# Optimization experiments

Measured on AMD Instinct MI355X. Metric: run time of the kernel, lower is better.

The kernel has to match this reference:

```python
import jax, jax.numpy as jnp
import numpy as np

B, T, L = 64, 60, 49
EMBED, HID, VOCAB = 768, 768, 10000


def setup_inputs() -> dict:
    key = jax.random.key(0)
    ks = jax.random.split(key, 17)
    def n(k, shape, s=1.0):
        return jax.random.normal(k, shape, dtype=jnp.float32) * s
    W = 0.02  # param init scale
    return {
        "x": n(ks[0], (B, T, 2 * EMBED)),
        "hiddens": n(ks[1], (B, T, HID)),
        "cells": n(ks[2], (B, T, HID)),
        "G": n(ks[3], (B, L, HID)),
        "H": n(ks[4], (B, L, HID)),
        # Sentinel params (bias=False)
        "W_sx": n(ks[5], (HID, 2 * EMBED), W),
        "W_sh": n(ks[6], (HID, HID), W),
        # SwitchableAttention params
        "W_ax": n(ks[7], (HID, 2 * EMBED), W),
        "W_ah": n(ks[8], (HID, HID), W),
        "W_ag": n(ks[9], (HID, HID), W),
        "w_switch": n(ks[10], (1, HID), W),
        # Atten (adaptive attention) params, bias=False
        "Wv": n(ks[11], (L, HID), W),
        "Wg": n(ks[12], (L, HID), W),
        "Ws": n(ks[13], (L, HID), W),
        "wh": n(ks[14], (1, L), W),
        # output MLP
        "W_mlp": n(ks[15], (VOCAB, HID), W),
        "b_mlp": jnp.zeros((VOCAB,), dtype=jnp.float32),
    }


def reference(x, hiddens, cells, G, H, W_sx, W_sh, W_ax, W_ah, W_ag,
              w_switch, Wv, Wg, Ws, wh, W_mlp, b_mlp):
    # Dropout layers are treated as identity (eval mode).
    b, t, _ = x.shape
    # h_{t-1}: zero initial hidden prepended, last step dropped
    h0 = jnp.zeros((b, 1, HID), dtype=hiddens.dtype)
    hiddens_t_1 = jnp.concatenate([h0, hiddens[:, :-1, :]], axis=1)

    # Sentinel gate: sigmoid(Wx x + Wh h_{t-1}) * tanh(c_t)
    gate = jax.nn.sigmoid(jnp.einsum('bte,he->bth', x, W_sx)
                          + jnp.einsum('btk,hk->bth', hiddens_t_1, W_sh))
    s_t = gate * jnp.tanh(cells)  # [B,T,HID]

    # SwitchableAttention: gate between visual H and guidance G per region,
    # conditioned on pooled word context x.
    q = jnp.einsum('bte,he->bth', x, W_ax).mean(axis=1)  # [B,HID]
    sH = jnp.einsum('blh,oh->blo', jnp.tanh(jnp.einsum('blh,kh->blk', H, W_ah) + q[:, None, :]), w_switch)  # [B,L,1]
    sG = jnp.einsum('blh,oh->blo', jnp.tanh(jnp.einsum('blh,kh->blk', G, W_ag) + q[:, None, :]), w_switch)  # [B,L,1]
    switch_weights = jax.nn.softmax(jnp.concatenate([sH, sG], axis=-1), axis=-1)  # [B,L,2]
    V = switch_weights[..., 0:1] * H + switch_weights[..., 1:2] * G  # [B,L,HID]

    # Adaptive attention (Atten): spatial attention + visual sentinel
    pv = jnp.einsum('blh,kh->blk', V, Wv)        # [B,L,49]
    pg = jnp.einsum('bth,kh->btk', hiddens, Wg)  # [B,T,49]
    z_t = jnp.einsum('btlk,ok->btlo', jnp.tanh(pv[:, None, :, :] + pg[:, :, None, :]), wh)[..., 0]  # [B,T,L]
    alpha = jax.nn.softmax(z_t, axis=-1)  # [B,T,L]
    z_s = jnp.einsum('btk,ok->bto', jnp.tanh(jnp.einsum('bth,kh->btk', s_t, Ws) + pg), wh)  # [B,T,1]
    alpha_hat = jax.nn.softmax(jnp.concatenate([z_t, z_s], axis=-1), axis=-1)  # [B,T,L+1]
    beta = alpha_hat[..., -1:]  # [B,T,1]
    c_t = jnp.einsum('btl,blh->bth', alpha, V)
    c_hat = beta * s_t + (1.0 - beta) * c_t

    scores = jnp.einsum('bth,vh->btv', c_hat + hiddens, W_mlp) + b_mlp  # [B,T,VOCAB]
    return scores, alpha, beta, switch_weights
```

## Files before the change

kernel.cpp:

```cpp
#include <hip/hip_runtime.h>

#define BB 64
#define TT 60
#define LL 49
#define HID 768
#define E2 1536
#define VOC 10000
#define BT (BB*TT)
#define BL (BB*LL)
#define NPAD_MLP 10240
#define NPAD_S 128

typedef __bf16 bf16x8 __attribute__((ext_vector_type(8)));
typedef float f32x4 __attribute__((ext_vector_type(4)));

__device__ __forceinline__ unsigned short f2bf(float f) {
  union { float f; unsigned int u; } v; v.f = f;
  unsigned int u = v.u;
  return (unsigned short)((u + 0x7fffu + ((u >> 16) & 1u)) >> 16);
}
__device__ __forceinline__ float bf2f(unsigned short h) {
  union { unsigned int u; float f; } v; v.u = ((unsigned int)h) << 16;
  return v.f;
}
__device__ __forceinline__ float fast_tanh(float x) {
  float e = __expf(2.f * x);
  return 1.f - 2.f / (e + 1.f);
}
__device__ __forceinline__ float fast_sigmoid(float x) {
  return 1.f / (1.f + __expf(-x));
}

#define NSEG 14
#define CHUNK4 2048
struct SegT {
  const float* src;
  unsigned short* dst;
  int n4;
  int nrows;
  int mode;
  int blk0;
};
struct SegTable { SegT s[NSEG]; };

__global__ __launch_bounds__(256) void k_convall(SegTable tab) {
  int b = blockIdx.x;
  int si = 0;
#pragma unroll
  for (int i = 1; i < NSEG; ++i) si += (b >= tab.s[i].blk0);
  SegT sg = tab.s[si];
  int lb = b - sg.blk0;
  int end = (lb + 1) * CHUNK4; end = end < sg.n4 ? end : sg.n4;
  for (int i = lb * CHUNK4 + threadIdx.x; i < end; i += 256) {
    ushort4 o; o.x = o.y = o.z = o.w = 0;
    if (sg.mode == 0) {
      float4 v = ((const float4*)sg.src)[i];
      o.x = f2bf(v.x); o.y = f2bf(v.y); o.z = f2bf(v.z); o.w = f2bf(v.w);
    } else if (sg.mode == 1) {
      int row = i / 192;
      if (row < sg.nrows) {
        float4 v = ((const float4*)sg.src)[i];
        o.x = f2bf(v.x); o.y = f2bf(v.y); o.z = f2bf(v.z); o.w = f2bf(v.w);
      }
    } else {
      int bt = i / 192;
      if (bt % TT != 0) {
        float4 v = ((const float4*)sg.src)[i - 192];
        o.x = f2bf(v.x); o.y = f2bf(v.y); o.z = f2bf(v.z); o.w = f2bf(v.w);
      }
    }
    ((ushort4*)sg.dst)[i] = o;
  }
}

__global__ __launch_bounds__(256) void k_xmean(const float* __restrict__ x,
                                               unsigned short* __restrict__ xm) {
  int b = blockIdx.x / 6;
  int c = (blockIdx.x % 6) * 256 + threadIdx.x;
  float s = 0.f;
  for (int t = 0; t < TT; ++t) s += x[((size_t)b * TT + t) * E2 + c];
  xm[(size_t)b * E2 + c] = f2bf(s * (1.f / 60.f));
}

struct SSeg {
  const unsigned short* A; const unsigned short* B; float* C;
  int M, Nout, K, nMblk, blk0;
};
#define NSSEG 3
struct SSegTable { SSeg s[NSSEG]; };

__global__ __launch_bounds__(256) void gemm_bt_seg(SSegTable tab)
{
  __shared__ __attribute__((aligned(16))) unsigned short As[128*32];
  __shared__ __attribute__((aligned(16))) unsigned short Bs[128*32];
  const int tid  = threadIdx.x;
  const int lane = tid & 63;
  const int wave = tid >> 6;

  const int nwg = gridDim.x;
  const int id  = blockIdx.x;
  const int q = nwg >> 3, r = nwg & 7;
  const int xcd = id & 7, lo = id >> 3;
  const int wgid = (xcd < r ? xcd * (q + 1) : r * (q + 1) + (xcd - r) * q) + lo;

  int si = 0;
#pragma unroll
  for (int i = 1; i < NSSEG; ++i) si += (wgid >= tab.s[i].blk0);
  const SSeg sg = tab.s[si];
  const int lwg = wgid - sg.blk0;
  const int mb = lwg % sg.nMblk;
  const int nb = lwg / sg.nMblk;
  const int M = sg.M, Nout = sg.Nout, K = sg.K;
  const unsigned short* __restrict__ A  = sg.A;
  const unsigned short* __restrict__ Bw = sg.B;
  float* __restrict__ C = sg.C;
  const int m0 = mb * 128;
  const int n0 = nb * 128;
  const int wm = (wave >> 1) * 64;
  const int wn = (wave & 1) * 64;

  f32x4 acc[4][4];
#pragma unroll
  for (int i = 0; i < 4; ++i)
#pragma unroll
    for (int j = 0; j < 4; ++j) acc[i][j] = f32x4{0.f, 0.f, 0.f, 0.f};

  const int lrow = lane & 15;
  const int kb   = (lane >> 4) * 8;

  for (int k0 = 0; k0 < K; k0 += 32) {
    __syncthreads();
#pragma unroll
    for (int p = 0; p < 2; ++p) {
      int slot = p * 256 + wave * 64 + lane;
      int row = slot >> 2, c8 = slot & 3;
      int ar = m0 + row; ar = ar < M ? ar : (M - 1);
      const unsigned short* asrc = A + (size_t)ar * K + k0 + c8 * 8;
      __builtin_amdgcn_global_load_lds(
          (const __attribute__((address_space(1))) void*)asrc,
          (__attribute__((address_space(3))) void*)&As[(p * 256 + wave * 64) * 8],
          16, 0, 0);
      const unsigned short* bsrc = Bw + (size_t)(n0 + row) * K + k0 + c8 * 8;
      __builtin_amdgcn_global_load_lds(
          (const __attribute__((address_space(1))) void*)bsrc,
          (__attribute__((address_space(3))) void*)&Bs[(p * 256 + wave * 64) * 8],
          16, 0, 0);
    }
    __syncthreads();

    bf16x8 av[4], bv[4];
#pragma unroll
    for (int i = 0; i < 4; ++i)
      av[i] = *(const bf16x8*)&As[(wm + i * 16 + lrow) * 32 + kb];
#pragma unroll
    for (int j = 0; j < 4; ++j)
      bv[j] = *(const bf16x8*)&Bs[(wn + j * 16 + lrow) * 32 + kb];
#pragma unroll
    for (int i = 0; i < 4; ++i)
#pragma unroll
      for (int j = 0; j < 4; ++j)
        acc[i][j] = __builtin_amdgcn_mfma_f32_16x16x32_bf16(av[i], bv[j], acc[i][j], 0, 0, 0);
  }

  const int cr = (lane >> 4) * 4;
  const int cc = lane & 15;
#pragma unroll
  for (int i = 0; i < 4; ++i) {
    int row0 = m0 + wm + i * 16 + cr;
#pragma unroll
    for (int j = 0; j < 4; ++j) {
      int col = n0 + wn + j * 16 + cc;
      if (col < Nout) {
#pragma unroll
        for (int r2 = 0; r2 < 4; ++r2) {
          int row = row0 + r2;
          if (row < M) C[(size_t)row * Nout + col] = acc[i][j][r2];
        }
      }
    }
  }
}

#define BARR() do { asm volatile("" ::: "memory"); __builtin_amdgcn_s_barrier(); \
                    asm volatile("" ::: "memory"); } while (0)
#define VM2() asm volatile("s_waitcnt vmcnt(2)" ::: "memory")
#define VM0() asm volatile("s_waitcnt vmcnt(0)" ::: "memory")

#define STAGE_OP(ct, op, kt) do {                                               \
  int k0_ = (kt) * 32;                                                          \
  _Pragma("unroll")                                                             \
  for (int l_ = 0; l_ < 2; ++l_) {                                              \
    int rr_ = l_ * 128 + sr0;                                                   \
    int ss_ = ssp ^ ((rr_ >> 1) & 3);                                           \
    int gr_ = (op) ? (n0 + rr_) : ((m0 + rr_) < M ? (m0 + rr_) : (M - 1));      \
    const unsigned short* src_ = ((op) ? Bw : Ap) + (size_t)gr_ * K + k0_ + ss_ * 8; \
    char* dst_ = smem + (ct) * 32768 + (op) * 16384 + l_ * 8192 + w * 1024;     \
    __builtin_amdgcn_global_load_lds(                                           \
        (const __attribute__((address_space(1))) void*)src_,                    \
        (__attribute__((address_space(3))) void*)dst_, 16, 0, 0);               \
  }                                                                             \
} while (0)

#define PHASE(c, JH, STAGE_STMT, VM_STMT) do {                                  \
  if ((JH) == 0) {                                                              \
    _Pragma("unroll")                                                           \
    for (int i_ = 0; i_ < 8; ++i_) {                                            \
      int rr_ = wm + i_ * 16 + lrow;                                            \
      int sp_ = cg ^ ((rr_ >> 1) & 3);                                          \
      afr[i_] = *(const bf16x8*)(smem + (c) * 32768 + rr_ * 64 + sp_ * 16);     \
    }                                                                           \
  }                                                                             \
  {                                                                             \
    int rb0_ = wn + ((JH) * 2) * 16 + lrow;                                     \
    int sb0_ = cg ^ ((rb0_ >> 1) & 3);                                          \
    bfr0 = *(const bf16x8*)(smem + (c) * 32768 + 16384 + rb0_ * 64 + sb0_ * 16); \
    int rb1_ = wn + ((JH) * 2 + 1) * 16 + lrow;                                 \
    int sb1_ = cg ^ ((rb1_ >> 1) & 3);                                          \
    bfr1 = *(const bf16x8*)(smem + (c) * 32768 + 16384 + rb1_ * 64 + sb1_ * 16); \
  }                                                                             \
  STAGE_STMT;                                                                   \
  BARR();                                                                       \
  asm volatile("s_waitcnt lgkmcnt(0)" ::: "memory");                            \
  __builtin_amdgcn_sched_barrier(0);                                            \
  __builtin_amdgcn_s_setprio(1);                                                \
  _Pragma("unroll")                                                             \
  for (int i_ = 0; i_ < 8; ++i_) {                                              \
    acc[i_][(JH) * 2]     = __builtin_amdgcn_mfma_f32_16x16x32_bf16(afr[i_], bfr0, acc[i_][(JH) * 2], 0, 0, 0);     \
    acc[i_][(JH) * 2 + 1] = __builtin_amdgcn_mfma_f32_16x16x32_bf16(afr[i_], bfr1, acc[i_][(JH) * 2 + 1], 0, 0, 0); \
  }                                                                             \
  __builtin_amdgcn_s_setprio(0);                                                \
  VM_STMT;                                                                      \
  BARR();                                                                       \
} while (0)

struct GSeg {
  const unsigned short* A; const unsigned short* B; float* C;
  const float* bias;
  int M, Nout, K, nMblk, blk0;
};
#define NGSEG 5
struct GSegTable { GSeg s[NGSEG]; };

__global__ __launch_bounds__(512, 2) void gemm8p(GSegTable tab)
{
  extern __shared__ char smem[];
  const int tid  = threadIdx.x;
  const int lane = tid & 63;
  const int w    = tid >> 6;
  const int lrow = lane & 15;
  const int cg   = lane >> 4;
  const int sr0  = w * 16 + (lane >> 2);
  const int ssp  = lane & 3;

  const int nwg = gridDim.x;
  const int id  = blockIdx.x;
  const int q = nwg >> 3, r = nwg & 7;
  const int xcd = id & 7, lo = id >> 3;
  const int wgid = (xcd < r ? xcd * (q + 1) : r * (q + 1) + (xcd - r) * q) + lo;

  int si = 0;
#pragma unroll
  for (int i = 1; i < NGSEG; ++i) si += (wgid >= tab.s[i].blk0);
  const GSeg sg = tab.s[si];
  const int lwg = wgid - sg.blk0;
  const int mb = lwg % sg.nMblk;
  const int nb = lwg / sg.nMblk;
  const int M = sg.M, Nout = sg.Nout, K = sg.K;
  const unsigned short* __restrict__ Ap = sg.A;
  const unsigned short* __restrict__ Bw = sg.B;
  float* __restrict__ C = sg.C;
  const float* __restrict__ bias = sg.bias;

  const int m0 = mb * 256;
  const int n0 = nb * 256;
  const int wm = (w >> 2) * 128;
  const int wn = (w & 3) * 64;

  f32x4 acc[8][4];
#pragma unroll
  for (int i = 0; i < 8; ++i)
#pragma unroll
    for (int j = 0; j < 4; ++j) acc[i][j] = f32x4{0.f, 0.f, 0.f, 0.f};
  bf16x8 afr[8];
  bf16x8 bfr0, bfr1;

  const int NT = K >> 5;

  STAGE_OP(0, 0, 0);
  STAGE_OP(0, 1, 0);
  STAGE_OP(1, 0, 1);
  VM2();
  BARR();

  for (int kt = 0; kt < NT - 2; ++kt) {
    const int c = kt & 1;
    PHASE(c, 0, STAGE_OP(c ^ 1, 1, kt + 1), ;);
    PHASE(c, 1, STAGE_OP(c, 0, kt + 2), VM2(););
  }
  {
    const int kt = NT - 2;
    const int c = kt & 1;
    PHASE(c, 0, STAGE_OP(c ^ 1, 1, NT - 1), ;);
    PHASE(c, 1, ;, VM0(););
  }
  {
    const int c = (NT - 1) & 1;
    PHASE(c, 0, ;, ;);
    PHASE(c, 1, ;, ;);
  }

#pragma unroll
  for (int i = 0; i < 8; ++i) {
    int row0 = m0 + wm + i * 16 + (lane >> 4) * 4;
#pragma unroll
    for (int j = 0; j < 4; ++j) {
      int col = n0 + wn + j * 16 + (lane & 15);
      if (col < Nout) {
        float badd = bias ? bias[col] : 0.f;
#pragma unroll
        for (int r2 = 0; r2 < 4; ++r2) {
          int row = row0 + r2;
          if (row < M) C[(size_t)row * Nout + col] = acc[i][j][r2] + badd;
        }
      }
    }
  }
}

__global__ void k_st(const float* __restrict__ XS, const float* __restrict__ HS,
                     const float* __restrict__ cells, unsigned short* __restrict__ stbf, int n) {
  int i = blockIdx.x * blockDim.x + threadIdx.x;
  int stride = gridDim.x * blockDim.x;
  for (; i < n; i += stride) {
    float pre = XS[i] + HS[i];
    float v = fast_sigmoid(pre) * fast_tanh(cells[i]);
    stbf[i] = f2bf(v);
  }
}

__global__ __launch_bounds__(256) void k_switch(
    const float* __restrict__ AH, const float* __restrict__ AG,
    const float* __restrict__ q, const float* __restrict__ wsw,
    const float* __restrict__ H, const float* __restrict__ G,
    unsigned short* __restrict__ Vbf, float* __restrict__ sw_out)
{
  int bl = blockIdx.x;
  int b = bl / LL;
  int tid = threadIdx.x;
  float aH = 0.f, aG = 0.f;
  for (int h = tid; h < HID; h += 256) {
    float qv = q[b * HID + h], w = wsw[h];
    aH += fast_tanh(AH[(size_t)bl * HID + h] + qv) * w;
    aG += fast_tanh(AG[(size_t)bl * HID + h] + qv) * w;
  }
#pragma unroll
  for (int off = 32; off > 0; off >>= 1) {
    aH += __shfl_down(aH, off);
    aG += __shfl_down(aG, off);
  }
  __shared__ float redH[4], redG[4];
  int lane = tid & 63, wave = tid >> 6;
  if (lane == 0) { redH[wave] = aH; redG[wave] = aG; }
  __syncthreads();
  float sH = redH[0] + redH[1] + redH[2] + redH[3];
  float sG = redG[0] + redG[1] + redG[2] + redG[3];
  float m = fmaxf(sH, sG);
  float e0 = __expf(sH - m), e1 = __expf(sG - m);
  float inv = 1.f / (e0 + e1);
  float sw0 = e0 * inv, sw1 = e1 * inv;
  if (tid == 0) { sw_out[bl * 2] = sw0; sw_out[bl * 2 + 1] = sw1; }
  for (int h = tid; h < HID; h += 256) {
    float v = sw0 * H[(size_t)bl * HID + h] + sw1 * G[(size_t)bl * HID + h];
    Vbf[(size_t)bl * HID + h] = f2bf(v);
  }
}

__global__ __launch_bounds__(256) void k_attn(
    const float* __restrict__ PV, const float* __restrict__ PG,
    const float* __restrict__ SS, const float* __restrict__ wh,
    const unsigned short* __restrict__ stbf, const unsigned short* __restrict__ Vbf,
    const float* __restrict__ hiddens,
    float* __restrict__ alpha_out, float* __restrict__ beta_out,
    unsigned short* __restrict__ chh)
{
  const int TG = 4;
  int b  = blockIdx.x / (TT / TG);
  int t0 = (blockIdx.x % (TT / TG)) * TG;
  int tid = threadIdx.x;
  __shared__ float pg_s[TG][LL], wh_s[LL], zz[TG][LL + 1], alpha_s[TG][LL], beta_sh[TG];

  if (tid < LL) wh_s[tid] = wh[tid];
  if (tid < TG * LL) {
    int tt = tid / LL, k = tid - tt * LL;
    pg_s[tt][k] = PG[(size_t)(b * TT + t0 + tt) * 64 + k];
  }
  __syncthreads();

  if (tid < TG * (LL + 1)) {
    int tt = tid / (LL + 1), l = tid - tt * (LL + 1);
    const float* src = (l < LL) ? &PV[((size_t)b * LL + l) * 64]
                                : &SS[(size_t)(b * TT + t0 + tt) * 64];
    float acc = 0.f;
    for (int k = 0; k < LL; ++k) acc += fast_tanh(src[k] + pg_s[tt][k]) * wh_s[k];
    zz[tt][l] = acc;
  }
  __syncthreads();

  if (tid < TG) {
    int tt = tid, bt = b * TT + t0 + tt;
    float mx = -1e30f;
    for (int l = 0; l < LL; ++l) mx = fmaxf(mx, zz[tt][l]);
    float sum = 0.f;
    for (int l = 0; l < LL; ++l) { float e = __expf(zz[tt][l] - mx); alpha_s[tt][l] = e; sum += e; }
    float inv = 1.f / sum;
    for (int l = 0; l < LL; ++l) {
      alpha_s[tt][l] *= inv;
      alpha_out[(size_t)bt * LL + l] = alpha_s[tt][l];
    }
    float mx2 = fmaxf(mx, zz[tt][LL]);
    float s2 = 0.f;
    for (int l = 0; l <= LL; ++l) s2 += __expf(zz[tt][l] - mx2);
    float bet = __expf(zz[tt][LL] - mx2) / s2;
    beta_sh[tt] = bet;
    beta_out[bt] = bet;
  }
  __syncthreads();

  for (int h = tid; h < HID; h += 256) {
    float ct[TG] = {0.f, 0.f, 0.f, 0.f};
    for (int l = 0; l < LL; ++l) {
      float v = bf2f(Vbf[((size_t)b * LL + l) * HID + h]);
#pragma unroll
      for (int tt = 0; tt < TG; ++tt) ct[tt] += alpha_s[tt][l] * v;
    }
#pragma unroll
    for (int tt = 0; tt < TG; ++tt) {
      int bt = b * TT + t0 + tt;
      float bet = beta_sh[tt];
      float s = bf2f(stbf[(size_t)bt * HID + h]);
      float chat = bet * s + (1.f - bet) * ct[tt];
      chh[(size_t)bt * HID + h] = f2bf(chat + hiddens[(size_t)bt * HID + h]);
    }
  }
}

static inline int nblk(long n) {
  long g = (n + 255) / 256;
  if (g > 8192) g = 8192;
  return (int)g;
}

extern "C" void kernel_launch(void* const* d_in, const int* in_sizes, int n_in,
                              void* d_out, int out_size, void* d_ws, size_t ws_size,
                              hipStream_t stream)
{
  const float* x       = (const float*)d_in[0];
  const float* hiddens = (const float*)d_in[1];
  const float* cells   = (const float*)d_in[2];
  const float* G       = (const float*)d_in[3];
  const float* H       = (const float*)d_in[4];
  const float* W_sx    = (const float*)d_in[5];
  const float* W_sh    = (const float*)d_in[6];
  const float* W_ax    = (const float*)d_in[7];
  const float* W_ah    = (const float*)d_in[8];
  const float* W_ag    = (const float*)d_in[9];
  const float* w_sw    = (const float*)d_in[10];
  const float* Wv      = (const float*)d_in[11];
  const float* Wg      = (const float*)d_in[12];
  const float* Ws      = (const float*)d_in[13];
  const float* wh      = (const float*)d_in[14];
  const float* W_mlp   = (const float*)d_in[15];
  const float* b_mlp   = (const float*)d_in[16];

  float* scores = (float*)d_out;
  float* alpha  = scores + (size_t)BT * VOC;
  float* beta   = alpha + (size_t)BT * LL;
  float* swout  = beta + BT;

  char* wsp = (char*)d_ws;
  size_t off = 0;
  auto alloc = [&](size_t bytes) -> char* {
    char* p = wsp + off;
    off += (bytes + 255) & ~(size_t)255;
    return p;
  };

  unsigned short* xbf    = (unsigned short*)alloc((size_t)BT * E2 * 2);
  unsigned short* wsa    = (unsigned short*)alloc((size_t)E2 * E2 * 2);
  unsigned short* hprev  = (unsigned short*)alloc((size_t)BT * HID * 2);
  unsigned short* wshb   = (unsigned short*)alloc((size_t)HID * HID * 2);
  unsigned short* wahb   = (unsigned short*)alloc((size_t)HID * HID * 2);
  unsigned short* wagb   = (unsigned short*)alloc((size_t)HID * HID * 2);
  unsigned short* Hbf    = (unsigned short*)alloc((size_t)BL * HID * 2);
  unsigned short* Gbf    = (unsigned short*)alloc((size_t)BL * HID * 2);
  unsigned short* hidbf  = (unsigned short*)alloc((size_t)BT * HID * 2);
  unsigned short* wvb    = (unsigned short*)alloc((size_t)NPAD_S * HID * 2);
  unsigned short* wgb    = (unsigned short*)alloc((size_t)NPAD_S * HID * 2);
  unsigned short* wsb    = (unsigned short*)alloc((size_t)NPAD_S * HID * 2);
  unsigned short* wmlpb  = (unsigned short*)alloc((size_t)NPAD_MLP * HID * 2);
  unsigned short* Vbf    = (unsigned short*)alloc((size_t)BL * HID * 2);
  unsigned short* stbf   = (unsigned short*)alloc((size_t)BT * HID * 2);
  unsigned short* chh    = (unsigned short*)alloc((size_t)BT * HID * 2);
  unsigned short* xmbf   = (unsigned short*)alloc((size_t)BB * E2 * 2);
  float* XS = (float*)alloc((size_t)BT * HID * 4);
  float* HS = (float*)alloc((size_t)BT * HID * 4);
  float* AH = (float*)alloc((size_t)BL * HID * 4);
  float* AG = (float*)alloc((size_t)BL * HID * 4);
  float* qb = (float*)alloc((size_t)BB * HID * 4);
  float* PV = (float*)alloc((size_t)BL * 64 * 4);
  float* PG = (float*)alloc((size_t)BT * 64 * 4);
  float* SS = (float*)alloc((size_t)BT * 64 * 4);
  (void)ws_size; (void)in_sizes; (void)n_in; (void)out_size;

  SegTable tab;
  int blk = 0, si = 0;
  auto seg = [&](const float* s, unsigned short* d, int n4, int nrows, int mode) {
    tab.s[si].src = s; tab.s[si].dst = d; tab.s[si].n4 = n4;
    tab.s[si].nrows = nrows; tab.s[si].mode = mode; tab.s[si].blk0 = blk;
    blk += (n4 + CHUNK4 - 1) / CHUNK4; ++si;
  };
  seg(W_sx, wsa,                        HID * E2 / 4, 0, 0);
  seg(W_ax, wsa + (size_t)HID * E2,     HID * E2 / 4, 0, 0);
  seg(x, xbf,                           BT * E2 / 4, 0, 0);
  seg(hiddens, hprev,                   BT * HID / 4, 0, 2);
  seg(W_sh, wshb,                       HID * HID / 4, 0, 0);
  seg(W_ah, wahb,                       HID * HID / 4, 0, 0);
  seg(W_ag, wagb,                       HID * HID / 4, 0, 0);
  seg(H, Hbf,                           BL * HID / 4, 0, 0);
  seg(G, Gbf,                           BL * HID / 4, 0, 0);
  seg(hiddens, hidbf,                   BT * HID / 4, 0, 0);
  seg(Wv, wvb,                          NPAD_S * HID / 4, LL, 1);
  seg(Wg, wgb,                          NPAD_S * HID / 4, LL, 1);
  seg(Ws, wsb,                          NPAD_S * HID / 4, LL, 1);
  seg(W_mlp, wmlpb,                     NPAD_MLP * HID / 4, VOC, 1);
  k_convall<<<blk, 256, 0, stream>>>(tab);

  k_xmean<<<BB * 6, 256, 0, stream>>>(x, xmbf);

  GSegTable gt;
  int gblk = 0, gi = 0;
  auto gseg = [&](const unsigned short* A, const unsigned short* B, float* C,
                  const float* bias, int M, int N, int K, int nMblk, int nNblk) {
    gt.s[gi].A = A; gt.s[gi].B = B; gt.s[gi].C = C; gt.s[gi].bias = bias;
    gt.s[gi].M = M; gt.s[gi].Nout = N; gt.s[gi].K = K; gt.s[gi].nMblk = nMblk;
    gt.s[gi].blk0 = gblk;
    gblk += nMblk * nNblk; ++gi;
  };
  gseg(xbf,   wsa,                      XS, nullptr, BT, HID, E2,  15, 3);
  gseg(hprev, wshb,                     HS, nullptr, BT, HID, HID, 15, 3);
  gseg(Hbf,   wahb,                     AH, nullptr, BL, HID, HID, 13, 3);
  gseg(Gbf,   wagb,                     AG, nullptr, BL, HID, HID, 13, 3);
  gseg(xmbf,  wsa + (size_t)HID * E2,   qb, nullptr, BB, HID, E2,  1,  3);
  gemm8p<<<gblk, 512, 65536, stream>>>(gt);

  k_st<<<nblk((long)BT * HID), 256, 0, stream>>>(XS, HS, cells, stbf, BT * HID);
  k_switch<<<BL, 256, 0, stream>>>(AH, AG, qb, w_sw, H, G, Vbf, swout);

  SSegTable st;
  st.s[0] = SSeg{Vbf,   wvb, PV, BL, 64, HID, 25, 0};
  st.s[1] = SSeg{hidbf, wgb, PG, BT, 64, HID, 30, 25};
  st.s[2] = SSeg{stbf,  wsb, SS, BT, 64, HID, 30, 55};
  gemm_bt_seg<<<85, 256, 0, stream>>>(st);

  k_attn<<<BB * (TT / 4), 256, 0, stream>>>(PV, PG, SS, wh, stbf, Vbf, hiddens,
                                            alpha, beta, chh);

  GSegTable gs;
  for (int i = 0; i < NGSEG; ++i) { gs.s[i] = gt.s[i]; gs.s[i].blk0 = 0x7fffffff; }
  gs.s[0] = GSeg{chh, wmlpb, scores, b_mlp, BT, VOC, HID, 15, 0};
  gemm8p<<<15 * 40, 512, 65536, stream>>>(gs);
}
```

Baseline: 311.3 us.

## Switch gemm8p to triple-buffered LDS pipeline with templated row clamping

Moves the main GEMM kernel from a double-buffered to a triple-buffered shared-memory pipeline. Both A and B tiles are now prefetched two k-steps ahead, the wait count is relaxed, and one barrier per phase is dropped. A template flag removes the row clamp and bounds check for the MLP GEMM, whose M is an exact multiple of the tile. Shared memory per block grows to 96KB, which may limit how many blocks fit per CU despite the two-block launch bound.

```diff
diff --git a/kernel.cpp b/kernel.cpp
--- a/kernel.cpp
+++ b/kernel.cpp
@@ -183,50 +183,54 @@
 
 #define BARR() do { asm volatile("" ::: "memory"); __builtin_amdgcn_s_barrier(); \
                     asm volatile("" ::: "memory"); } while (0)
-#define VM2() asm volatile("s_waitcnt vmcnt(2)" ::: "memory")
+#define VM4() asm volatile("s_waitcnt vmcnt(4)" ::: "memory")
 #define VM0() asm volatile("s_waitcnt vmcnt(0)" ::: "memory")
 
-#define STAGE_OP(ct, op, kt) do {                                               \
+#define STAGE1(bufi, op, kt) do {                                               \
   int k0_ = (kt) * 32;                                                          \
   _Pragma("unroll")                                                             \
   for (int l_ = 0; l_ < 2; ++l_) {                                              \
     int rr_ = l_ * 128 + sr0;                                                   \
     int ss_ = ssp ^ ((rr_ >> 1) & 3);                                           \
-    int gr_ = (op) ? (n0 + rr_) : ((m0 + rr_) < M ? (m0 + rr_) : (M - 1));      \
+    int gr_;                                                                    \
+    if (op) gr_ = n0 + rr_;                                                     \
+    else    gr_ = CLAMP ? ((m0 + rr_) < M ? (m0 + rr_) : (M - 1)) : (m0 + rr_); \
     const unsigned short* src_ = ((op) ? Bw : Ap) + (size_t)gr_ * K + k0_ + ss_ * 8; \
-    char* dst_ = smem + (ct) * 32768 + (op) * 16384 + l_ * 8192 + w * 1024;     \
+    char* dst_ = smem + (bufi) * 32768 + (op) * 16384 + l_ * 8192 + w * 1024;   \
     __builtin_amdgcn_global_load_lds(                                           \
         (const __attribute__((address_space(1))) void*)src_,                    \
         (__attribute__((address_space(3))) void*)dst_, 16, 0, 0);               \
   }                                                                             \
 } while (0)
 
-#define PHASE(c, JH, STAGE_STMT, VM_STMT) do {                                  \
-  if ((JH) == 0) {                                                              \
-    _Pragma("unroll")                                                           \
-    for (int i_ = 0; i_ < 8; ++i_) {                                            \
-      int rr_ = wm + i_ * 16 + lrow;                                            \
-      int sp_ = cg ^ ((rr_ >> 1) & 3);                                          \
-      afr[i_] = *(const bf16x8*)(smem + (c) * 32768 + rr_ * 64 + sp_ * 16);     \
-    }                                                                           \
-  }                                                                             \
-  {                                                                             \
-    int rb0_ = wn + ((JH) * 2) * 16 + lrow;                                     \
-    int sb0_ = cg ^ ((rb0_ >> 1) & 3);                                          \
-    bfr0 = *(const bf16x8*)(smem + (c) * 32768 + 16384 + rb0_ * 64 + sb0_ * 16); \
-    int rb1_ = wn + ((JH) * 2 + 1) * 16 + lrow;                                 \
-    int sb1_ = cg ^ ((rb1_ >> 1) & 3);                                          \
-    bfr1 = *(const bf16x8*)(smem + (c) * 32768 + 16384 + rb1_ * 64 + sb1_ * 16); \
-  }                                                                             \
+#define LDA(bufi, row) (*(const bf16x8*)(smem + (bufi) * 32768 + (row) * 64 + (cg ^ (((row) >> 1) & 3)) * 16))
+#define LDB(bufi, row) (*(const bf16x8*)(smem + (bufi) * 32768 + 16384 + (row) * 64 + (cg ^ (((row) >> 1) & 3)) * 16))
+
+#define PH0(bufi, STAGE_STMT) do {                                              \
   STAGE_STMT;                                                                   \
-  BARR();                                                                       \
-  asm volatile("s_waitcnt lgkmcnt(0)" ::: "memory");                            \
-  __builtin_amdgcn_sched_barrier(0);                                            \
+  bfr0 = LDB(bufi, wn + lrow);                                                  \
+  bfr1 = LDB(bufi, wn + 16 + lrow);                                             \
+  _Pragma("unroll")                                                             \
+  for (int i_ = 0; i_ < 8; ++i_) afr[i_] = LDA(bufi, wm + i_ * 16 + lrow);      \
   __builtin_amdgcn_s_setprio(1);                                                \
   _Pragma("unroll")                                                             \
   for (int i_ = 0; i_ < 8; ++i_) {                                              \
-    acc[i_][(JH) * 2]     = __builtin_amdgcn_mfma_f32_16x16x32_bf16(afr[i_], bfr0, acc[i_][(JH) * 2], 0, 0, 0);     \
-    acc[i_][(JH) * 2 + 1] = __builtin_amdgcn_mfma_f32_16x16x32_bf16(afr[i_], bfr1, acc[i_][(JH) * 2 + 1], 0, 0, 0); \
+    acc[i_][0] = __builtin_amdgcn_mfma_f32_16x16x32_bf16(afr[i_], bfr0, acc[i_][0], 0, 0, 0); \
+    acc[i_][1] = __builtin_amdgcn_mfma_f32_16x16x32_bf16(afr[i_], bfr1, acc[i_][1], 0, 0, 0); \
+  }                                                                             \
+  __builtin_amdgcn_s_setprio(0);                                                \
+  BARR();                                                                       \
+} while (0)
+
+#define PH1(bufi, STAGE_STMT, VM_STMT) do {                                     \
+  STAGE_STMT;                                                                   \
+  bfr0 = LDB(bufi, wn + 32 + lrow);                                             \
+  bfr1 = LDB(bufi, wn + 48 + lrow);                                             \
+  __builtin_amdgcn_s_setprio(1);                                                \
+  _Pragma("unroll")                                                             \
+  for (int i_ = 0; i_ < 8; ++i_) {                                              \
+    acc[i_][2] = __builtin_amdgcn_mfma_f32_16x16x32_bf16(afr[i_], bfr0, acc[i_][2], 0, 0, 0); \
+    acc[i_][3] = __builtin_amdgcn_mfma_f32_16x16x32_bf16(afr[i_], bfr1, acc[i_][3], 0, 0, 0); \
   }                                                                             \
   __builtin_amdgcn_s_setprio(0);                                                \
   VM_STMT;                                                                      \
@@ -241,6 +245,7 @@
 #define NGSEG 5
 struct GSegTable { GSeg s[NGSEG]; };
 
+template <bool CLAMP>
 __global__ __launch_bounds__(512, 2) void gemm8p(GSegTable tab)
 {
   extern __shared__ char smem[];
@@ -286,27 +291,32 @@
 
   const int NT = K >> 5;
 
-  STAGE_OP(0, 0, 0);
-  STAGE_OP(0, 1, 0);
-  STAGE_OP(1, 0, 1);
-  VM2();
+  STAGE1(0, 0, 0);
+  STAGE1(0, 1, 0);
+  STAGE1(1, 0, 1);
+  STAGE1(1, 1, 1);
+  VM4();
   BARR();
 
+  int b = 0;
   for (int kt = 0; kt < NT - 2; ++kt) {
-    const int c = kt & 1;
-    PHASE(c, 0, STAGE_OP(c ^ 1, 1, kt + 1), ;);
-    PHASE(c, 1, STAGE_OP(c, 0, kt + 2), VM2(););
-  }
+    int b2 = b + 2; if (b2 >= 3) b2 -= 3;
+    PH0(b, STAGE1(b2, 0, kt + 2));
+    PH1(b, STAGE1(b2, 1, kt + 2), VM4(););
+    ++b; if (b == 3) b = 0;
+  }
+  PH0(b, ;);
+  PH1(b, ;, VM0(););
+  ++b; if (b == 3) b = 0;
+  PH0(b, ;);
   {
-    const int kt = NT - 2;
-    const int c = kt & 1;
-    PHASE(c, 0, STAGE_OP(c ^ 1, 1, NT - 1), ;);
-    PHASE(c, 1, ;, VM0(););
-  }
-  {
-    const int c = (NT - 1) & 1;
-    PHASE(c, 0, ;, ;);
-    PHASE(c, 1, ;, ;);
+    bfr0 = LDB(b, wn + 32 + lrow);
+    bfr1 = LDB(b, wn + 48 + lrow);
+#pragma unroll
+    for (int i_ = 0; i_ < 8; ++i_) {
+      acc[i_][2] = __builtin_amdgcn_mfma_f32_16x16x32_bf16(afr[i_], bfr0, acc[i_][2], 0, 0, 0);
+      acc[i_][3] = __builtin_amdgcn_mfma_f32_16x16x32_bf16(afr[i_], bfr1, acc[i_][3], 0, 0, 0);
+    }
   }
 
 #pragma unroll
@@ -320,7 +330,7 @@
 #pragma unroll
         for (int r2 = 0; r2 < 4; ++r2) {
           int row = row0 + r2;
-          if (row < M) C[(size_t)row * Nout + col] = acc[i][j][r2] + badd;
+          if (!CLAMP || row < M) C[(size_t)row * Nout + col] = acc[i][j][r2] + badd;
         }
       }
     }
@@ -551,7 +561,7 @@
   gseg(Hbf,   wahb,                     AH, nullptr, BL, HID, HID, 13, 3);
   gseg(Gbf,   wagb,                     AG, nullptr, BL, HID, HID, 13, 3);
   gseg(xmbf,  wsa + (size_t)HID * E2,   qb, nullptr, BB, HID, E2,  1,  3);
-  gemm8p<<<gblk, 512, 65536, stream>>>(gt);
+  gemm8p<true><<<gblk, 512, 98304, stream>>>(gt);
 
   k_st<<<nblk((long)BT * HID), 256, 0, stream>>>(XS, HS, cells, stbf, BT * HID);
   k_switch<<<BL, 256, 0, stream>>>(AH, AG, qb, w_sw, H, G, Vbf, swout);
@@ -566,7 +576,7 @@
                                             alpha, beta, chh);
 
   GSegTable gs;
-  for (int i = 0; i < NGSEG; ++i) { gs.s[i] = gt.s[i]; gs.s[i].blk0 = 0x7fffffff; }
-  gs.s[0] = GSeg{chh, wmlpb, scores, b_mlp, BT, VOC, HID, 15, 0};
-  gemm8p<<<15 * 40, 512, 65536, stream>>>(gs);
-}
+  for (int i = 0; i < NGSEG; ++i) { gs.s[i].blk0 = 0x7fffffff; gs.s[i].A = chh; gs.s[i].B = wmlpb; gs.s[i].C = scores; gs.s[i].bias = b_mlp; gs.s[i].M = BT; gs.s[i].Nout = VOC; gs.s[i].K = HID; gs.s[i].nMblk = 15; }
+  gs.s[0].blk0 = 0;
+  gemm8p<false><<<15 * 40, 512, 98304, stream>>>(gs);
+}
```

Result: faster. 292.6 us (-6.0%).
